# Kernel optimization log

Hardware: AMD Instinct MI355X
Metric: run time of the kernel (lower is better)

The kernel has to match this reference:

```python
import jax, jax.numpy as jnp
import numpy as np

MARGIN = 0.5
CURV = 1.0
B, D = 8192, 128
N_CLASSES = 256


def setup_inputs() -> dict:
    key = jax.random.key(0)
    k1, k2, k3 = jax.random.split(key, 3)
    emb = jax.random.normal(k1, (B, D), dtype=jnp.float32)
    # project onto Poincare ball: random radii in (0, 0.8) so all norms < 1
    radii = 0.8 * jax.random.uniform(k2, (B, 1), dtype=jnp.float32)
    emb = emb / (jnp.linalg.norm(emb, axis=-1, keepdims=True) + 1e-6) * radii
    labels = jax.random.randint(k3, (B,), 0, N_CLASSES, dtype=jnp.int64)
    return {"embeddings": emb, "labels": labels}


def _poincare_dist_matrix(x, c):
    # d(x,y) = arccosh(1 + 2c||x-y||^2 / ((1-c||x||^2)(1-c||y||^2))) / sqrt(c)
    sq = jnp.sum(x * x, axis=-1)                       # (B,)
    gram = x @ x.T                                      # (B,B) GEMM
    d2 = jnp.maximum(sq[:, None] + sq[None, :] - 2.0 * gram, 0.0)
    denom = (1.0 - c * sq)[:, None] * (1.0 - c * sq)[None, :]
    arg = 1.0 + 2.0 * c * d2 / denom
    # clamp slightly above 1: arccosh grad is infinite at 1 (diagonal / identical pts)
    return jnp.arccosh(jnp.maximum(arg, 1.0 + 1e-7)) / jnp.sqrt(c)


def reference(embeddings, labels):
    dist = _poincare_dist_matrix(embeddings, CURV)      # (B,B)
    same = labels[:, None] == labels[None, :]
    eye = jnp.eye(labels.shape[0], dtype=bool)
    pos_mask = same & ~eye
    neg_mask = ~same
    has_pos = jnp.any(pos_mask, axis=1)
    has_neg = jnp.any(neg_mask, axis=1)
    valid = has_pos & has_neg
    d_pos = jnp.max(jnp.where(pos_mask, dist, -jnp.inf), axis=1)
    d_neg = jnp.min(jnp.where(neg_mask, dist, jnp.inf), axis=1)
    d_pos = jnp.where(has_pos, d_pos, 0.0)
    d_neg = jnp.where(has_neg, d_neg, 0.0)
    l = jnp.maximum(d_pos - d_neg + MARGIN, 0.0)
    l = jnp.where(valid, l, 0.0)
    cnt = jnp.sum(valid)
    return jnp.where(cnt > 0, jnp.sum(l) / jnp.maximum(cnt, 1), 0.0)
```

## Files before the change

kernel.cpp:

```cpp
#include <hip/hip_runtime.h>
#include <hip/hip_bf16.h>

typedef __attribute__((ext_vector_type(8))) __bf16 bf16x8;
typedef __attribute__((ext_vector_type(4))) float f32x4;
typedef unsigned short u16;
typedef unsigned int u32;

#define NB 8192
#define ND 128
#define NEGINF (-__builtin_inff())
#define POSINF (__builtin_inff())
#define ENC_NEGINF 0x007FFFFFu
#define ENC_POSINF 0xFF800000u

__device__ inline u16 f2b(float f){
  __hip_bfloat16 h = __float2bfloat16(f);
  return *reinterpret_cast<u16*>(&h);
}
__device__ inline u32 encf(float f){
  u32 b = __float_as_uint(f);
  return b ^ (0x80000000u | (u32)(((int)b) >> 31));
}
__device__ inline float decf(u32 u){
  return __uint_as_float(u ^ (0x80000000u | (u32)((~(int)u) >> 31)));
}

extern "C" __global__ __launch_bounds__(256)
void prep_k(const float* __restrict__ x, const int* __restrict__ lab,
            u16* __restrict__ xb, float4* __restrict__ colp,
            u32* __restrict__ ppos, u32* __restrict__ pneg)
{
  const int tid = blockIdx.x * 256 + threadIdx.x;
  const int row = tid >> 5;
  const int sub = tid & 31;
  const float4 v = reinterpret_cast<const float4*>(x)[row * 32 + sub];
  float s = v.x*v.x + v.y*v.y + v.z*v.z + v.w*v.w;
  #pragma unroll
  for (int m = 1; m < 32; m <<= 1) s += __shfl_xor(s, m, 32);
  ushort4 o;
  o.x = f2b(v.x); o.y = f2b(v.y); o.z = f2b(v.z); o.w = f2b(v.w);
  reinterpret_cast<ushort4*>(xb)[row * 32 + sub] = o;
  if (sub == 0){
    const float p = 1.0f / (1.0f - s);
    colp[row] = make_float4(s, p, s * p, __int_as_float(lab[row]));
  }
  if (sub == 1) ppos[row] = ENC_NEGINF;
  if (sub == 2) pneg[row] = ENC_POSINF;
}

extern "C" __global__ __launch_bounds__(256, 2)
void gram_k(const u16* __restrict__ xb, const float4* __restrict__ colp,
            u32* __restrict__ ppos, u32* __restrict__ pneg)
{
  __shared__ u16 Bt[128 * 128];
  const int wid  = threadIdx.x >> 6;
  const int lane = threadIdx.x & 63;
  const int m16  = lane & 15;
  const int quad = lane >> 4;

  int idx = (int)blockIdx.x;
  int bi = (int)((129.0f - sqrtf((float)(16641 - 8 * idx))) * 0.5f);
  while ((bi + 1) * (129 - (bi + 1)) / 2 <= idx) ++bi;
  while (bi * (129 - bi) / 2 > idx) --bi;
  const int bj = bi + (idx - bi * (129 - bi) / 2);
  const bool diag = (bi == bj);
  const int C0  = bj * 128;
  const int WR0 = bi * 128 + wid * 32;

  #pragma unroll
  for (int c = 0; c < 8; ++c){
    const int cc   = wid * 8 + c;
    const int brow = cc * 4 + quad;
    const int src  = m16 ^ (brow & 15);
    const u16* gsrc = xb + (C0 + brow) * ND + src * 8;
    __builtin_amdgcn_global_load_lds(
        (const __attribute__((address_space(1))) void*)gsrc,
        (__attribute__((address_space(3))) void*)(Bt + cc * 512), 16, 0, 0);
  }

  bf16x8 afrag[2][4];
  #pragma unroll
  for (int mt = 0; mt < 2; ++mt){
    const u16* arow = xb + (WR0 + mt*16 + m16) * ND;
    #pragma unroll
    for (int ks = 0; ks < 4; ++ks)
      afrag[mt][ks] = *reinterpret_cast<const bf16x8*>(arow + ks*32 + quad*8);
  }

  float sqi[8], pi[8]; int labi[8];
  #pragma unroll
  for (int mt = 0; mt < 2; ++mt)
    #pragma unroll
    for (int r = 0; r < 4; ++r){
      const float4 cp = colp[WR0 + mt*16 + quad*4 + r];
      sqi[mt*4+r]  = cp.x;
      pi[mt*4+r]   = cp.y;
      labi[mt*4+r] = __float_as_int(cp.w);
    }

  __syncthreads();

  f32x4 acc[2][8];
  #pragma unroll
  for (int mt = 0; mt < 2; ++mt)
    #pragma unroll
    for (int nt = 0; nt < 8; ++nt){
      f32x4 z = {0.f, 0.f, 0.f, 0.f};
      acc[mt][nt] = z;
    }

  #pragma unroll
  for (int ks = 0; ks < 4; ++ks){
    const int t = ks * 4 + quad;
    #pragma unroll
    for (int nt = 0; nt < 8; ++nt){
      const bf16x8 bfrag = *reinterpret_cast<const bf16x8*>(
          Bt + (nt*16 + m16) * 128 + ((t ^ m16) * 8));
      acc[0][nt] = __builtin_amdgcn_mfma_f32_16x16x32_bf16(afrag[0][ks], bfrag, acc[0][nt], 0, 0, 0);
      acc[1][nt] = __builtin_amdgcn_mfma_f32_16x16x32_bf16(afrag[1][ks], bfrag, acc[1][nt], 0, 0, 0);
    }
  }

  float vpos[8], vneg[8], cpos[8], cneg[8];
  #pragma unroll
  for (int i = 0; i < 8; ++i){
    vpos[i] = NEGINF; vneg[i] = POSINF;
    cpos[i] = NEGINF; cneg[i] = POSINF;
  }

  if (!diag){
    #pragma unroll
    for (int nt = 0; nt < 8; ++nt){
      const float4 cp = colp[C0 + nt*16 + m16];
      const float sqj  = cp.x;
      const float pj   = cp.y;
      const int   labj = __float_as_int(cp.w);
      #pragma unroll
      for (int mt = 0; mt < 2; ++mt)
        #pragma unroll
        for (int r = 0; r < 4; ++r){
          const int i = mt*4 + r;
          const float d2 = fmaf(-2.0f, acc[mt][nt][r], sqi[i] + sqj);
          const float ur = d2 * pj;
          const float uc = d2 * pi[i];
          const bool sm = (labi[i] == labj);
          vpos[i]  = fmaxf(vpos[i],  sm ? ur : NEGINF);
          vneg[i]  = fminf(vneg[i],  sm ? POSINF : ur);
          cpos[nt] = fmaxf(cpos[nt], sm ? uc : NEGINF);
          cneg[nt] = fminf(cneg[nt], sm ? POSINF : uc);
        }
    }
  } else {
    #pragma unroll
    for (int nt = 0; nt < 8; ++nt){
      const float4 cp = colp[C0 + nt*16 + m16];
      const float sqj  = cp.x;
      const float pj   = cp.y;
      const int   labj = __float_as_int(cp.w);
      const int colin  = nt*16 + m16;
      #pragma unroll
      for (int mt = 0; mt < 2; ++mt)
        #pragma unroll
        for (int r = 0; r < 4; ++r){
          const int i = mt*4 + r;
          const float d2 = fmaf(-2.0f, acc[mt][nt][r], sqi[i] + sqj);
          const float ur = d2 * pj;
          const bool sm = (labi[i] == labj);
          const bool dg = (colin == wid*32 + mt*16 + quad*4 + r);
          float ep = sm ? ur : NEGINF;
          ep = dg ? NEGINF : ep;
          vpos[i] = fmaxf(vpos[i], ep);
          vneg[i] = fminf(vneg[i], sm ? POSINF : ur);
        }
    }
  }

  #pragma unroll
  for (int i = 0; i < 8; ++i){
    #pragma unroll
    for (int m = 1; m < 16; m <<= 1){
      vpos[i] = fmaxf(vpos[i], __shfl_xor(vpos[i], m, 16));
      vneg[i] = fminf(vneg[i], __shfl_xor(vneg[i], m, 16));
    }
  }
  if (m16 == 0){
    #pragma unroll
    for (int i = 0; i < 8; ++i){
      const int row = WR0 + (i >> 2)*16 + quad*4 + (i & 3);
      atomicMax(ppos + row, encf(vpos[i]));
      atomicMin(pneg + row, encf(vneg[i]));
    }
  }

  if (!diag){
    #pragma unroll
    for (int nt = 0; nt < 8; ++nt){
      cpos[nt] = fmaxf(cpos[nt], __shfl_xor(cpos[nt], 16));
      cpos[nt] = fmaxf(cpos[nt], __shfl_xor(cpos[nt], 32));
      cneg[nt] = fminf(cneg[nt], __shfl_xor(cneg[nt], 16));
      cneg[nt] = fminf(cneg[nt], __shfl_xor(cneg[nt], 32));
    }
    float* cbP = reinterpret_cast<float*>(Bt);
    float* cbN = cbP + 512;
    __syncthreads();
    if (quad == 0){
      #pragma unroll
      for (int nt = 0; nt < 8; ++nt){
        cbP[wid*128 + nt*16 + m16] = cpos[nt];
        cbN[wid*128 + nt*16 + m16] = cneg[nt];
      }
    }
    __syncthreads();
    if (threadIdx.x < 128){
      const int c = threadIdx.x;
      float P = NEGINF, N = POSINF;
      #pragma unroll
      for (int w = 0; w < 4; ++w){
        P = fmaxf(P, cbP[w*128 + c]);
        N = fminf(N, cbN[w*128 + c]);
      }
      atomicMax(ppos + C0 + c, encf(P));
      atomicMin(pneg + C0 + c, encf(N));
    }
  }
}

extern "C" __global__ __launch_bounds__(128)
void fin1_k(const u32* __restrict__ ppos, const u32* __restrict__ pneg,
            const float4* __restrict__ colp, float2* __restrict__ bpart)
{
  const int row = blockIdx.x * 128 + threadIdx.x;
  const float up = decf(ppos[row]);
  const float un = decf(pneg[row]);
  const bool hp = (up > NEGINF);
  const bool hn = (un < POSINF);
  const float pr = colp[row].y;
  float dp = 0.0f, dn = 0.0f;
  if (hp){ float t = fmaxf(2.0f * up * pr, 1e-7f); dp = log1pf(t + sqrtf(t * (t + 2.0f))); }
  if (hn){ float t = fmaxf(2.0f * un * pr, 1e-7f); dn = log1pf(t + sqrtf(t * (t + 2.0f))); }
  float lsum = (hp && hn) ? fmaxf(dp - dn + 0.5f, 0.0f) : 0.0f;
  float lcnt = (hp && hn) ? 1.0f : 0.0f;
  #pragma unroll
  for (int m = 1; m < 64; m <<= 1){
    lsum += __shfl_xor(lsum, m, 64);
    lcnt += __shfl_xor(lcnt, m, 64);
  }
  __shared__ float2 s_p[2];
  if ((threadIdx.x & 63) == 0) s_p[threadIdx.x >> 6] = make_float2(lsum, lcnt);
  __syncthreads();
  if (threadIdx.x == 0)
    bpart[blockIdx.x] = make_float2(s_p[0].x + s_p[1].x, s_p[0].y + s_p[1].y);
}

extern "C" __global__ __launch_bounds__(64)
void fin2_k(const float2* __restrict__ bpart, float* __restrict__ out)
{
  float2 p = bpart[threadIdx.x];
  float s = p.x, c = p.y;
  #pragma unroll
  for (int m = 1; m < 64; m <<= 1){
    s += __shfl_xor(s, m, 64);
    c += __shfl_xor(c, m, 64);
  }
  if (threadIdx.x == 0) out[0] = (c > 0.0f) ? (s / c) : 0.0f;
}

extern "C" void kernel_launch(void* const* d_in, const int* in_sizes, int n_in,
                              void* d_out, int out_size, void* d_ws, size_t ws_size,
                              hipStream_t stream)
{
  const float* x  = (const float*)d_in[0];
  const int* lab  = (const int*)d_in[1];
  char* ws = (char*)d_ws;
  u16*    xb   = (u16*)ws;
  float4* colp = (float4*)(ws + (size_t)2*1024*1024);
  u32*    ppos = (u32*)(ws + (size_t)2*1024*1024 + 128*1024);
  u32*    pneg = (u32*)(ws + (size_t)2*1024*1024 + 160*1024);
  float2* bpart= (float2*)(ws + (size_t)2*1024*1024 + 192*1024);

  hipLaunchKernelGGL(prep_k, dim3(1024), dim3(256), 0, stream, x, lab, xb, colp, ppos, pneg);
  hipLaunchKernelGGL(gram_k, dim3(2080), dim3(256), 0, stream, xb, colp, ppos, pneg);
  hipLaunchKernelGGL(fin1_k, dim3(64), dim3(128), 0, stream, ppos, pneg, colp, bpart);
  hipLaunchKernelGGL(fin2_k, dim3(1), dim3(64), 0, stream, bpart, (float*)d_out);
}
```

Measured before the change: 105.6 us.

## Sort rows by label so most tiles skip positive-mask work; fuse finalization

Adds a single-block counting sort of rows by class. Embeddings are permuted so each 128-row tile spans a narrow label range, and tile pairs with disjoint class ranges take a cheaper path that tracks only negative minima, without label compares or positive max. The separate finalization kernels are folded into the gram kernel through a last-block-done atomic counter. The MFMA epilogue is split into two halves to reduce register pressure, and occupancy is raised to 3 blocks. This adds a serial single-block sort kernel plus a gather in prep, which adds launch latency and uncoalesced reads.

```diff
diff --git a/kernel.cpp b/kernel.cpp
--- a/kernel.cpp
+++ b/kernel.cpp
@@ -8,6 +8,7 @@
 
 #define NB 8192
 #define ND 128
+#define NBLK 2080
 #define NEGINF (-__builtin_inff())
 #define POSINF (__builtin_inff())
 #define ENC_NEGINF 0x007FFFFFu
@@ -24,48 +25,96 @@
 __device__ inline float decf(u32 u){
   return __uint_as_float(u ^ (0x80000000u | (u32)((~(int)u) >> 31)));
 }
+__device__ inline f32x4 mfma16(bf16x8 a, bf16x8 b, f32x4 c){
+  return __builtin_amdgcn_mfma_f32_16x16x32_bf16(a, b, c, 0, 0, 0);
+}
+
+extern "C" __global__ __launch_bounds__(256)
+void sort_k(const int* __restrict__ lab, int* __restrict__ srcOf,
+            u32* __restrict__ tileCls)
+{
+  __shared__ u32 hist[256], scan[256], startB[256], cnt[256];
+  __shared__ u16 clsS[NB];
+  const int t = threadIdx.x;
+  hist[t] = 0; cnt[t] = 0;
+  __syncthreads();
+  for (int r = t; r < NB; r += 256) atomicAdd(&hist[lab[r]], 1u);
+  __syncthreads();
+  scan[t] = hist[t];
+  __syncthreads();
+  #pragma unroll
+  for (int off = 1; off < 256; off <<= 1){
+    u32 add = (t >= off) ? scan[t - off] : 0u;
+    __syncthreads();
+    scan[t] += add;
+    __syncthreads();
+  }
+  startB[t] = scan[t] - hist[t];
+  __syncthreads();
+  for (int r = t; r < NB; r += 256){
+    const int c = lab[r];
+    const u32 pos = startB[c] + atomicAdd(&cnt[c], 1u);
+    srcOf[pos] = r;
+    clsS[pos] = (u16)c;
+  }
+  __syncthreads();
+  if (t < 64)
+    tileCls[t] = (u32)clsS[t * 128] | ((u32)clsS[t * 128 + 127] << 16);
+}
 
 extern "C" __global__ __launch_bounds__(256)
 void prep_k(const float* __restrict__ x, const int* __restrict__ lab,
+            const int* __restrict__ srcOf,
             u16* __restrict__ xb, float4* __restrict__ colp,
-            u32* __restrict__ ppos, u32* __restrict__ pneg)
+            u32* __restrict__ ppos, u32* __restrict__ pneg,
+            u32* __restrict__ done)
 {
-  const int tid = blockIdx.x * 256 + threadIdx.x;
-  const int row = tid >> 5;
-  const int sub = tid & 31;
-  const float4 v = reinterpret_cast<const float4*>(x)[row * 32 + sub];
-  float s = v.x*v.x + v.y*v.y + v.z*v.z + v.w*v.w;
-  #pragma unroll
-  for (int m = 1; m < 32; m <<= 1) s += __shfl_xor(s, m, 32);
-  ushort4 o;
-  o.x = f2b(v.x); o.y = f2b(v.y); o.z = f2b(v.z); o.w = f2b(v.w);
-  reinterpret_cast<ushort4*>(xb)[row * 32 + sub] = o;
-  if (sub == 0){
-    const float p = 1.0f / (1.0f - s);
-    colp[row] = make_float4(s, p, s * p, __int_as_float(lab[row]));
-  }
-  if (sub == 1) ppos[row] = ENC_NEGINF;
-  if (sub == 2) pneg[row] = ENC_POSINF;
-}
-
-extern "C" __global__ __launch_bounds__(256, 2)
+  const int R0 = blockIdx.x * 128;
+  const int rr  = threadIdx.x >> 5;
+  const int sub = threadIdx.x & 31;
+  for (int it = 0; it < 16; ++it){
+    const int s   = R0 + it * 8 + rr;
+    const int src = srcOf[s];
+    const float4 v = reinterpret_cast<const float4*>(x)[src * 32 + sub];
+    float ss = v.x*v.x + v.y*v.y + v.z*v.z + v.w*v.w;
+    #pragma unroll
+    for (int m = 1; m < 32; m <<= 1) ss += __shfl_xor(ss, m, 32);
+    ushort4 o;
+    o.x = f2b(v.x); o.y = f2b(v.y); o.z = f2b(v.z); o.w = f2b(v.w);
+    reinterpret_cast<ushort4*>(xb)[s * 32 + sub] = o;
+    if (sub == 0){
+      const float p = 1.0f / (1.0f - ss);
+      colp[s] = make_float4(ss, p, ss * p, __int_as_float(lab[src]));
+    }
+  }
+  if (threadIdx.x < 128) ppos[R0 + threadIdx.x] = ENC_NEGINF;
+  else                   pneg[R0 + threadIdx.x - 128] = ENC_POSINF;
+  if (blockIdx.x == 0 && threadIdx.x == 0) *done = 0u;
+}
+
+extern "C" __global__ __launch_bounds__(256, 3)
 void gram_k(const u16* __restrict__ xb, const float4* __restrict__ colp,
-            u32* __restrict__ ppos, u32* __restrict__ pneg)
+            const u32* __restrict__ tileCls,
+            u32* __restrict__ ppos, u32* __restrict__ pneg,
+            u32* __restrict__ done, float* __restrict__ out)
 {
   __shared__ u16 Bt[128 * 128];
+  __shared__ u32 s_last;
   const int wid  = threadIdx.x >> 6;
   const int lane = threadIdx.x & 63;
   const int m16  = lane & 15;
   const int quad = lane >> 4;
 
   int idx = (int)blockIdx.x;
-  int bi = (int)((129.0f - sqrtf((float)(16641 - 8 * idx))) * 0.5f);
-  while ((bi + 1) * (129 - (bi + 1)) / 2 <= idx) ++bi;
-  while (bi * (129 - bi) / 2 > idx) --bi;
-  const int bj = bi + (idx - bi * (129 - bi) / 2);
-  const bool diag = (bi == bj);
+  int bi0 = (int)((129.0f - sqrtf((float)(16641 - 8 * idx))) * 0.5f);
+  while ((bi0 + 1) * (129 - (bi0 + 1)) / 2 <= idx) ++bi0;
+  while (bi0 * (129 - bi0) / 2 > idx) --bi0;
+  const int bi = __builtin_amdgcn_readfirstlane(bi0);
+  const int bj = __builtin_amdgcn_readfirstlane(bi0 + (idx - bi0 * (129 - bi0) / 2));
   const int C0  = bj * 128;
   const int WR0 = bi * 128 + wid * 32;
+  const u32 tci = tileCls[bi], tcj = tileCls[bj];
+  const bool fat = ((tci >> 16) >= (tcj & 0xFFFFu));
 
   #pragma unroll
   for (int c = 0; c < 8; ++c){
@@ -87,182 +136,259 @@
       afrag[mt][ks] = *reinterpret_cast<const bf16x8*>(arow + ks*32 + quad*8);
   }
 
-  float sqi[8], pi[8]; int labi[8];
+  float sqi[8], pi[8];
   #pragma unroll
   for (int mt = 0; mt < 2; ++mt)
     #pragma unroll
     for (int r = 0; r < 4; ++r){
       const float4 cp = colp[WR0 + mt*16 + quad*4 + r];
-      sqi[mt*4+r]  = cp.x;
-      pi[mt*4+r]   = cp.y;
-      labi[mt*4+r] = __float_as_int(cp.w);
-    }
-
-  __syncthreads();
-
-  f32x4 acc[2][8];
-  #pragma unroll
-  for (int mt = 0; mt < 2; ++mt)
+      sqi[mt*4+r] = cp.x;
+      pi[mt*4+r]  = cp.y;
+    }
+
+  __syncthreads();
+
+  if (!fat){
+    float vneg[8], cneg[8];
+    #pragma unroll
+    for (int i = 0; i < 8; ++i){ vneg[i] = POSINF; cneg[i] = POSINF; }
+
+    #pragma unroll
+    for (int half = 0; half < 2; ++half){
+      float4 cpv[4];
+      #pragma unroll
+      for (int nt4 = 0; nt4 < 4; ++nt4)
+        cpv[nt4] = colp[C0 + (half*4 + nt4)*16 + m16];
+      f32x4 acc[2][4];
+      #pragma unroll
+      for (int mt = 0; mt < 2; ++mt)
+        #pragma unroll
+        for (int nt4 = 0; nt4 < 4; ++nt4){
+          f32x4 z = {0.f,0.f,0.f,0.f};
+          acc[mt][nt4] = z;
+        }
+      #pragma unroll
+      for (int ks = 0; ks < 4; ++ks){
+        const int t = ks * 4 + quad;
+        #pragma unroll
+        for (int nt4 = 0; nt4 < 4; ++nt4){
+          const int nt = half*4 + nt4;
+          const bf16x8 bfrag = *reinterpret_cast<const bf16x8*>(
+              Bt + (nt*16 + m16) * 128 + ((t ^ m16) * 8));
+          acc[0][nt4] = mfma16(afrag[0][ks], bfrag, acc[0][nt4]);
+          acc[1][nt4] = mfma16(afrag[1][ks], bfrag, acc[1][nt4]);
+        }
+      }
+      #pragma unroll
+      for (int nt4 = 0; nt4 < 4; ++nt4){
+        const int nt = half*4 + nt4;
+        const float sqj = cpv[nt4].x, pj = cpv[nt4].y;
+        #pragma unroll
+        for (int mt = 0; mt < 2; ++mt)
+          #pragma unroll
+          for (int r = 0; r < 4; ++r){
+            const int i = mt*4 + r;
+            const float d2 = fmaf(-2.0f, acc[mt][nt4][r], sqi[i] + sqj);
+            vneg[i]  = fminf(vneg[i],  d2 * pj);
+            cneg[nt] = fminf(cneg[nt], d2 * pi[i]);
+          }
+      }
+    }
+    #pragma unroll
+    for (int i = 0; i < 8; ++i)
+      #pragma unroll
+      for (int m = 1; m < 16; m <<= 1)
+        vneg[i] = fminf(vneg[i], __shfl_xor(vneg[i], m, 16));
+    if (m16 == 0){
+      #pragma unroll
+      for (int i = 0; i < 8; ++i){
+        const int row = WR0 + (i >> 2)*16 + quad*4 + (i & 3);
+        atomicMin(pneg + row, encf(vneg[i]));
+      }
+    }
     #pragma unroll
     for (int nt = 0; nt < 8; ++nt){
-      f32x4 z = {0.f, 0.f, 0.f, 0.f};
-      acc[mt][nt] = z;
-    }
-
-  #pragma unroll
-  for (int ks = 0; ks < 4; ++ks){
-    const int t = ks * 4 + quad;
-    #pragma unroll
-    for (int nt = 0; nt < 8; ++nt){
-      const bf16x8 bfrag = *reinterpret_cast<const bf16x8*>(
-          Bt + (nt*16 + m16) * 128 + ((t ^ m16) * 8));
-      acc[0][nt] = __builtin_amdgcn_mfma_f32_16x16x32_bf16(afrag[0][ks], bfrag, acc[0][nt], 0, 0, 0);
-      acc[1][nt] = __builtin_amdgcn_mfma_f32_16x16x32_bf16(afrag[1][ks], bfrag, acc[1][nt], 0, 0, 0);
-    }
-  }
-
-  float vpos[8], vneg[8], cpos[8], cneg[8];
-  #pragma unroll
-  for (int i = 0; i < 8; ++i){
-    vpos[i] = NEGINF; vneg[i] = POSINF;
-    cpos[i] = NEGINF; cneg[i] = POSINF;
-  }
-
-  if (!diag){
-    #pragma unroll
-    for (int nt = 0; nt < 8; ++nt){
-      const float4 cp = colp[C0 + nt*16 + m16];
-      const float sqj  = cp.x;
-      const float pj   = cp.y;
-      const int   labj = __float_as_int(cp.w);
-      #pragma unroll
-      for (int mt = 0; mt < 2; ++mt)
-        #pragma unroll
-        for (int r = 0; r < 4; ++r){
-          const int i = mt*4 + r;
-          const float d2 = fmaf(-2.0f, acc[mt][nt][r], sqi[i] + sqj);
-          const float ur = d2 * pj;
-          const float uc = d2 * pi[i];
-          const bool sm = (labi[i] == labj);
-          vpos[i]  = fmaxf(vpos[i],  sm ? ur : NEGINF);
-          vneg[i]  = fminf(vneg[i],  sm ? POSINF : ur);
-          cpos[nt] = fmaxf(cpos[nt], sm ? uc : NEGINF);
-          cneg[nt] = fminf(cneg[nt], sm ? POSINF : uc);
-        }
-    }
-  } else {
-    #pragma unroll
-    for (int nt = 0; nt < 8; ++nt){
-      const float4 cp = colp[C0 + nt*16 + m16];
-      const float sqj  = cp.x;
-      const float pj   = cp.y;
-      const int   labj = __float_as_int(cp.w);
-      const int colin  = nt*16 + m16;
-      #pragma unroll
-      for (int mt = 0; mt < 2; ++mt)
-        #pragma unroll
-        for (int r = 0; r < 4; ++r){
-          const int i = mt*4 + r;
-          const float d2 = fmaf(-2.0f, acc[mt][nt][r], sqi[i] + sqj);
-          const float ur = d2 * pj;
-          const bool sm = (labi[i] == labj);
-          const bool dg = (colin == wid*32 + mt*16 + quad*4 + r);
-          float ep = sm ? ur : NEGINF;
-          ep = dg ? NEGINF : ep;
-          vpos[i] = fmaxf(vpos[i], ep);
-          vneg[i] = fminf(vneg[i], sm ? POSINF : ur);
-        }
-    }
-  }
-
-  #pragma unroll
-  for (int i = 0; i < 8; ++i){
-    #pragma unroll
-    for (int m = 1; m < 16; m <<= 1){
-      vpos[i] = fmaxf(vpos[i], __shfl_xor(vpos[i], m, 16));
-      vneg[i] = fminf(vneg[i], __shfl_xor(vneg[i], m, 16));
-    }
-  }
-  if (m16 == 0){
-    #pragma unroll
-    for (int i = 0; i < 8; ++i){
-      const int row = WR0 + (i >> 2)*16 + quad*4 + (i & 3);
-      atomicMax(ppos + row, encf(vpos[i]));
-      atomicMin(pneg + row, encf(vneg[i]));
-    }
-  }
-
-  if (!diag){
-    #pragma unroll
-    for (int nt = 0; nt < 8; ++nt){
-      cpos[nt] = fmaxf(cpos[nt], __shfl_xor(cpos[nt], 16));
-      cpos[nt] = fmaxf(cpos[nt], __shfl_xor(cpos[nt], 32));
       cneg[nt] = fminf(cneg[nt], __shfl_xor(cneg[nt], 16));
       cneg[nt] = fminf(cneg[nt], __shfl_xor(cneg[nt], 32));
     }
-    float* cbP = reinterpret_cast<float*>(Bt);
-    float* cbN = cbP + 512;
+    float* cbN = reinterpret_cast<float*>(Bt);
     __syncthreads();
     if (quad == 0){
       #pragma unroll
-      for (int nt = 0; nt < 8; ++nt){
-        cbP[wid*128 + nt*16 + m16] = cpos[nt];
+      for (int nt = 0; nt < 8; ++nt)
         cbN[wid*128 + nt*16 + m16] = cneg[nt];
-      }
     }
     __syncthreads();
     if (threadIdx.x < 128){
       const int c = threadIdx.x;
-      float P = NEGINF, N = POSINF;
-      #pragma unroll
-      for (int w = 0; w < 4; ++w){
-        P = fmaxf(P, cbP[w*128 + c]);
-        N = fminf(N, cbN[w*128 + c]);
-      }
-      atomicMax(ppos + C0 + c, encf(P));
+      float N = POSINF;
+      #pragma unroll
+      for (int w = 0; w < 4; ++w) N = fminf(N, cbN[w*128 + c]);
       atomicMin(pneg + C0 + c, encf(N));
     }
-  }
-}
-
-extern "C" __global__ __launch_bounds__(128)
-void fin1_k(const u32* __restrict__ ppos, const u32* __restrict__ pneg,
-            const float4* __restrict__ colp, float2* __restrict__ bpart)
-{
-  const int row = blockIdx.x * 128 + threadIdx.x;
-  const float up = decf(ppos[row]);
-  const float un = decf(pneg[row]);
-  const bool hp = (up > NEGINF);
-  const bool hn = (un < POSINF);
-  const float pr = colp[row].y;
-  float dp = 0.0f, dn = 0.0f;
-  if (hp){ float t = fmaxf(2.0f * up * pr, 1e-7f); dp = log1pf(t + sqrtf(t * (t + 2.0f))); }
-  if (hn){ float t = fmaxf(2.0f * un * pr, 1e-7f); dn = log1pf(t + sqrtf(t * (t + 2.0f))); }
-  float lsum = (hp && hn) ? fmaxf(dp - dn + 0.5f, 0.0f) : 0.0f;
-  float lcnt = (hp && hn) ? 1.0f : 0.0f;
-  #pragma unroll
-  for (int m = 1; m < 64; m <<= 1){
-    lsum += __shfl_xor(lsum, m, 64);
-    lcnt += __shfl_xor(lcnt, m, 64);
-  }
-  __shared__ float2 s_p[2];
-  if ((threadIdx.x & 63) == 0) s_p[threadIdx.x >> 6] = make_float2(lsum, lcnt);
-  __syncthreads();
+  } else {
+    const bool diag = (bi == bj);
+    int labi[8];
+    const float* colpF = reinterpret_cast<const float*>(colp);
+    #pragma unroll
+    for (int mt = 0; mt < 2; ++mt)
+      #pragma unroll
+      for (int r = 0; r < 4; ++r)
+        labi[mt*4+r] = __float_as_int(colpF[(WR0 + mt*16 + quad*4 + r)*4 + 3]);
+
+    float vpos[8], vneg[8], cpos[8], cneg[8];
+    #pragma unroll
+    for (int i = 0; i < 8; ++i){
+      vpos[i] = NEGINF; vneg[i] = POSINF;
+      cpos[i] = NEGINF; cneg[i] = POSINF;
+    }
+
+    #pragma unroll
+    for (int half = 0; half < 2; ++half){
+      float4 cpv[4];
+      #pragma unroll
+      for (int nt4 = 0; nt4 < 4; ++nt4)
+        cpv[nt4] = colp[C0 + (half*4 + nt4)*16 + m16];
+      f32x4 acc[2][4];
+      #pragma unroll
+      for (int mt = 0; mt < 2; ++mt)
+        #pragma unroll
+        for (int nt4 = 0; nt4 < 4; ++nt4){
+          f32x4 z = {0.f,0.f,0.f,0.f};
+          acc[mt][nt4] = z;
+        }
+      #pragma unroll
+      for (int ks = 0; ks < 4; ++ks){
+        const int t = ks * 4 + quad;
+        #pragma unroll
+        for (int nt4 = 0; nt4 < 4; ++nt4){
+          const int nt = half*4 + nt4;
+          const bf16x8 bfrag = *reinterpret_cast<const bf16x8*>(
+              Bt + (nt*16 + m16) * 128 + ((t ^ m16) * 8));
+          acc[0][nt4] = mfma16(afrag[0][ks], bfrag, acc[0][nt4]);
+          acc[1][nt4] = mfma16(afrag[1][ks], bfrag, acc[1][nt4]);
+        }
+      }
+      #pragma unroll
+      for (int nt4 = 0; nt4 < 4; ++nt4){
+        const int nt = half*4 + nt4;
+        const float sqj  = cpv[nt4].x;
+        const float pj   = cpv[nt4].y;
+        const int   labj = __float_as_int(cpv[nt4].w);
+        if (!diag){
+          #pragma unroll
+          for (int mt = 0; mt < 2; ++mt)
+            #pragma unroll
+            for (int r = 0; r < 4; ++r){
+              const int i = mt*4 + r;
+              const float d2 = fmaf(-2.0f, acc[mt][nt4][r], sqi[i] + sqj);
+              const float ur = d2 * pj;
+              const float uc = d2 * pi[i];
+              const bool sm = (labi[i] == labj);
+              vpos[i]  = fmaxf(vpos[i],  sm ? ur : NEGINF);
+              vneg[i]  = fminf(vneg[i],  sm ? POSINF : ur);
+              cpos[nt] = fmaxf(cpos[nt], sm ? uc : NEGINF);
+              cneg[nt] = fminf(cneg[nt], sm ? POSINF : uc);
+            }
+        } else {
+          const int colin = nt*16 + m16;
+          #pragma unroll
+          for (int mt = 0; mt < 2; ++mt)
+            #pragma unroll
+            for (int r = 0; r < 4; ++r){
+              const int i = mt*4 + r;
+              const float d2 = fmaf(-2.0f, acc[mt][nt4][r], sqi[i] + sqj);
+              const float ur = d2 * pj;
+              const bool sm = (labi[i] == labj);
+              const bool dg = (colin == wid*32 + mt*16 + quad*4 + r);
+              float ep = sm ? ur : NEGINF;
+              ep = dg ? NEGINF : ep;
+              vpos[i] = fmaxf(vpos[i], ep);
+              vneg[i] = fminf(vneg[i], sm ? POSINF : ur);
+            }
+        }
+      }
+    }
+    #pragma unroll
+    for (int i = 0; i < 8; ++i)
+      #pragma unroll
+      for (int m = 1; m < 16; m <<= 1){
+        vpos[i] = fmaxf(vpos[i], __shfl_xor(vpos[i], m, 16));
+        vneg[i] = fminf(vneg[i], __shfl_xor(vneg[i], m, 16));
+      }
+    if (m16 == 0){
+      #pragma unroll
+      for (int i = 0; i < 8; ++i){
+        const int row = WR0 + (i >> 2)*16 + quad*4 + (i & 3);
+        atomicMax(ppos + row, encf(vpos[i]));
+        atomicMin(pneg + row, encf(vneg[i]));
+      }
+    }
+    if (!diag){
+      #pragma unroll
+      for (int nt = 0; nt < 8; ++nt){
+        cpos[nt] = fmaxf(cpos[nt], __shfl_xor(cpos[nt], 16));
+        cpos[nt] = fmaxf(cpos[nt], __shfl_xor(cpos[nt], 32));
+        cneg[nt] = fminf(cneg[nt], __shfl_xor(cneg[nt], 16));
+        cneg[nt] = fminf(cneg[nt], __shfl_xor(cneg[nt], 32));
+      }
+      float* cbP = reinterpret_cast<float*>(Bt);
+      float* cbN = cbP + 512;
+      __syncthreads();
+      if (quad == 0){
+        #pragma unroll
+        for (int nt = 0; nt < 8; ++nt){
+          cbP[wid*128 + nt*16 + m16] = cpos[nt];
+          cbN[wid*128 + nt*16 + m16] = cneg[nt];
+        }
+      }
+      __syncthreads();
+      if (threadIdx.x < 128){
+        const int c = threadIdx.x;
+        float P = NEGINF, N = POSINF;
+        #pragma unroll
+        for (int w = 0; w < 4; ++w){
+          P = fmaxf(P, cbP[w*128 + c]);
+          N = fminf(N, cbN[w*128 + c]);
+        }
+        atomicMax(ppos + C0 + c, encf(P));
+        atomicMin(pneg + C0 + c, encf(N));
+      }
+    }
+  }
+
+  __threadfence();
   if (threadIdx.x == 0)
-    bpart[blockIdx.x] = make_float2(s_p[0].x + s_p[1].x, s_p[0].y + s_p[1].y);
-}
-
-extern "C" __global__ __launch_bounds__(64)
-void fin2_k(const float2* __restrict__ bpart, float* __restrict__ out)
-{
-  float2 p = bpart[threadIdx.x];
-  float s = p.x, c = p.y;
-  #pragma unroll
-  for (int m = 1; m < 64; m <<= 1){
-    s += __shfl_xor(s, m, 64);
-    c += __shfl_xor(c, m, 64);
-  }
-  if (threadIdx.x == 0) out[0] = (c > 0.0f) ? (s / c) : 0.0f;
+    s_last = (atomicAdd(done, 1u) == (u32)(NBLK - 1)) ? 1u : 0u;
+  __syncthreads();
+  if (s_last){
+    __threadfence();
+    float lsum = 0.0f, lcnt = 0.0f;
+    for (int r = (int)threadIdx.x; r < NB; r += 256){
+      const float up = decf(atomicMax(ppos + r, 0u));
+      const float un = decf(atomicMin(pneg + r, 0xFFFFFFFFu));
+      const bool hp = (up > NEGINF);
+      const bool hn = (un < POSINF);
+      const float pr = colp[r].y;
+      float dp = 0.0f, dn = 0.0f;
+      if (hp){ float t = fmaxf(2.0f * up * pr, 1e-7f); dp = log1pf(t + sqrtf(t * (t + 2.0f))); }
+      if (hn){ float t = fmaxf(2.0f * un * pr, 1e-7f); dn = log1pf(t + sqrtf(t * (t + 2.0f))); }
+      if (hp && hn){ lsum += fmaxf(dp - dn + 0.5f, 0.0f); lcnt += 1.0f; }
+    }
+    #pragma unroll
+    for (int m = 1; m < 64; m <<= 1){
+      lsum += __shfl_xor(lsum, m, 64);
+      lcnt += __shfl_xor(lcnt, m, 64);
+    }
+    float2* sp = reinterpret_cast<float2*>(Bt);
+    if ((threadIdx.x & 63) == 0) sp[threadIdx.x >> 6] = make_float2(lsum, lcnt);
+    __syncthreads();
+    if (threadIdx.x == 0){
+      const float S = sp[0].x + sp[1].x + sp[2].x + sp[3].x;
+      const float C = sp[0].y + sp[1].y + sp[2].y + sp[3].y;
+      out[0] = (C > 0.0f) ? (S / C) : 0.0f;
+    }
+  }
 }
 
 extern "C" void kernel_launch(void* const* d_in, const int* in_sizes, int n_in,
@@ -272,14 +398,17 @@
   const float* x  = (const float*)d_in[0];
   const int* lab  = (const int*)d_in[1];
   char* ws = (char*)d_ws;
-  u16*    xb   = (u16*)ws;
-  float4* colp = (float4*)(ws + (size_t)2*1024*1024);
-  u32*    ppos = (u32*)(ws + (size_t)2*1024*1024 + 128*1024);
-  u32*    pneg = (u32*)(ws + (size_t)2*1024*1024 + 160*1024);
-  float2* bpart= (float2*)(ws + (size_t)2*1024*1024 + 192*1024);
-
-  hipLaunchKernelGGL(prep_k, dim3(1024), dim3(256), 0, stream, x, lab, xb, colp, ppos, pneg);
-  hipLaunchKernelGGL(gram_k, dim3(2080), dim3(256), 0, stream, xb, colp, ppos, pneg);
-  hipLaunchKernelGGL(fin1_k, dim3(64), dim3(128), 0, stream, ppos, pneg, colp, bpart);
-  hipLaunchKernelGGL(fin2_k, dim3(1), dim3(64), 0, stream, bpart, (float*)d_out);
-}
+  u16*    xb    = (u16*)ws;
+  float4* colp  = (float4*)(ws + (size_t)2*1024*1024);
+  u32*    ppos  = (u32*)(ws + (size_t)2*1024*1024 + 128*1024);
+  u32*    pneg  = (u32*)(ws + (size_t)2*1024*1024 + 160*1024);
+  int*    srcOf = (int*)(ws + (size_t)2*1024*1024 + 192*1024);
+  u32*    tileCls = (u32*)(ws + (size_t)2*1024*1024 + 224*1024);
+  u32*    done  = (u32*)(ws + (size_t)2*1024*1024 + 225*1024);
+
+  hipLaunchKernelGGL(sort_k, dim3(1), dim3(256), 0, stream, lab, srcOf, tileCls);
+  hipLaunchKernelGGL(prep_k, dim3(64), dim3(256), 0, stream,
+                     x, lab, srcOf, xb, colp, ppos, pneg, done);
+  hipLaunchKernelGGL(gram_k, dim3(NBLK), dim3(256), 0, stream,
+                     xb, colp, tileCls, ppos, pneg, done, (float*)d_out);
+}
```

After: 259.2 us. 2.45x slower.

## Fuse prep, gram and finalize kernels into one launch with last-block reduction

Applied to the files above, without the earlier changes.

Replaces the four-kernel pipeline (bf16 prep, gram, two finalize passes) with a memset plus a single fused kernel. Each tile block converts its own fp32 rows to bf16 and computes norms on the fly, and the last block to finish does the final loss reduction. The scaled distance is now folded symmetrically as d2*pi*pj, and the atomics are skipped for infinite values. This removes launch overhead and the intermediate bf16 buffer, at the cost of redundant conversion and norm work for every tile and a serial finalize done by one block.

```diff
diff --git a/kernel.cpp b/kernel.cpp
--- a/kernel.cpp
+++ b/kernel.cpp
@@ -7,16 +7,10 @@
 typedef unsigned int u32;
 
 #define NB 8192
-#define ND 128
+#define NBLK 2080
 #define NEGINF (-__builtin_inff())
 #define POSINF (__builtin_inff())
-#define ENC_NEGINF 0x007FFFFFu
-#define ENC_POSINF 0xFF800000u
-
-__device__ inline u16 f2b(float f){
-  __hip_bfloat16 h = __float2bfloat16(f);
-  return *reinterpret_cast<u16*>(&h);
-}
+
 __device__ inline u32 encf(float f){
   u32 b = __float_as_uint(f);
   return b ^ (0x80000000u | (u32)(((int)b) >> 31));
@@ -24,81 +18,92 @@
 __device__ inline float decf(u32 u){
   return __uint_as_float(u ^ (0x80000000u | (u32)((~(int)u) >> 31)));
 }
-
-extern "C" __global__ __launch_bounds__(256)
-void prep_k(const float* __restrict__ x, const int* __restrict__ lab,
-            u16* __restrict__ xb, float4* __restrict__ colp,
-            u32* __restrict__ ppos, u32* __restrict__ pneg)
-{
-  const int tid = blockIdx.x * 256 + threadIdx.x;
-  const int row = tid >> 5;
-  const int sub = tid & 31;
-  const float4 v = reinterpret_cast<const float4*>(x)[row * 32 + sub];
-  float s = v.x*v.x + v.y*v.y + v.z*v.z + v.w*v.w;
-  #pragma unroll
-  for (int m = 1; m < 32; m <<= 1) s += __shfl_xor(s, m, 32);
-  ushort4 o;
-  o.x = f2b(v.x); o.y = f2b(v.y); o.z = f2b(v.z); o.w = f2b(v.w);
-  reinterpret_cast<ushort4*>(xb)[row * 32 + sub] = o;
-  if (sub == 0){
-    const float p = 1.0f / (1.0f - s);
-    colp[row] = make_float4(s, p, s * p, __int_as_float(lab[row]));
-  }
-  if (sub == 1) ppos[row] = ENC_NEGINF;
-  if (sub == 2) pneg[row] = ENC_POSINF;
+__device__ inline f32x4 mfma16(bf16x8 a, bf16x8 b, f32x4 c){
+  return __builtin_amdgcn_mfma_f32_16x16x32_bf16(a, b, c, 0, 0, 0);
+}
+__device__ inline ushort4 cvt4(float4 a){
+  union { ushort4 s; __hip_bfloat162 h[2]; } u;
+  u.h[0] = __float22bfloat162_rn(make_float2(a.x, a.y));
+  u.h[1] = __float22bfloat162_rn(make_float2(a.z, a.w));
+  return u.s;
+}
+__device__ inline bf16x8 cvt8(float4 a, float4 b){
+  union { bf16x8 v; __hip_bfloat162 h[4]; } u;
+  u.h[0] = __float22bfloat162_rn(make_float2(a.x, a.y));
+  u.h[1] = __float22bfloat162_rn(make_float2(a.z, a.w));
+  u.h[2] = __float22bfloat162_rn(make_float2(b.x, b.y));
+  u.h[3] = __float22bfloat162_rn(make_float2(b.z, b.w));
+  return u.v;
 }
 
 extern "C" __global__ __launch_bounds__(256, 2)
-void gram_k(const u16* __restrict__ xb, const float4* __restrict__ colp,
-            u32* __restrict__ ppos, u32* __restrict__ pneg)
+void fused_k(const float* __restrict__ x, const int* __restrict__ lab,
+             u32* __restrict__ pm, u32* __restrict__ nm,
+             u32* __restrict__ done, float* __restrict__ out)
 {
   __shared__ u16 Bt[128 * 128];
-  const int wid  = threadIdx.x >> 6;
-  const int lane = threadIdx.x & 63;
+  __shared__ float sqA[128], pA[128], sqB[128], pB[128];
+  __shared__ int labA[128], labB[128];
+  __shared__ u32 s_last;
+  __shared__ float2 s_fin[4];
+
+  const int tid  = threadIdx.x;
+  const int wid  = tid >> 6;
+  const int lane = tid & 63;
   const int m16  = lane & 15;
   const int quad = lane >> 4;
 
   int idx = (int)blockIdx.x;
-  int bi = (int)((129.0f - sqrtf((float)(16641 - 8 * idx))) * 0.5f);
-  while ((bi + 1) * (129 - (bi + 1)) / 2 <= idx) ++bi;
-  while (bi * (129 - bi) / 2 > idx) --bi;
-  const int bj = bi + (idx - bi * (129 - bi) / 2);
+  int bi0 = (int)((129.0f - sqrtf((float)(16641 - 8 * idx))) * 0.5f);
+  while ((bi0 + 1) * (129 - (bi0 + 1)) / 2 <= idx) ++bi0;
+  while (bi0 * (129 - bi0) / 2 > idx) --bi0;
+  const int bi = bi0;
+  const int bj = bi0 + (idx - bi0 * (129 - bi0) / 2);
   const bool diag = (bi == bj);
-  const int C0  = bj * 128;
-  const int WR0 = bi * 128 + wid * 32;
-
-  #pragma unroll
-  for (int c = 0; c < 8; ++c){
-    const int cc   = wid * 8 + c;
-    const int brow = cc * 4 + quad;
-    const int src  = m16 ^ (brow & 15);
-    const u16* gsrc = xb + (C0 + brow) * ND + src * 8;
-    __builtin_amdgcn_global_load_lds(
-        (const __attribute__((address_space(1))) void*)gsrc,
-        (__attribute__((address_space(3))) void*)(Bt + cc * 512), 16, 0, 0);
+  const int R0 = bi * 128, C0 = bj * 128;
+  const int WR0 = R0 + wid * 32;
+
+  const int rr = tid >> 5, sub = tid & 31;
+  for (int pp = 0; pp < 16; ++pp){
+    const int r = pp * 8 + rr;
+    const float4 va = reinterpret_cast<const float4*>(x)[(R0 + r) * 32 + sub];
+    float sa = va.x*va.x + va.y*va.y + va.z*va.z + va.w*va.w;
+    #pragma unroll
+    for (int m = 1; m < 32; m <<= 1) sa += __shfl_xor(sa, m, 32);
+    const float4 vb = reinterpret_cast<const float4*>(x)[(C0 + r) * 32 + sub];
+    float sb = vb.x*vb.x + vb.y*vb.y + vb.z*vb.z + vb.w*vb.w;
+    #pragma unroll
+    for (int m = 1; m < 32; m <<= 1) sb += __shfl_xor(sb, m, 32);
+    if (sub == 0){
+      sqA[r] = sa; pA[r] = 1.0f / (1.0f - sa);
+      sqB[r] = sb; pB[r] = 1.0f / (1.0f - sb);
+    }
+    if (sub == 1) labA[r] = lab[R0 + r];
+    if (sub == 2) labB[r] = lab[C0 + r];
+    reinterpret_cast<ushort4*>(Bt)[r*32 + (((sub>>1) ^ (r & 15)) << 1) + (sub & 1)] = cvt4(vb);
   }
 
   bf16x8 afrag[2][4];
   #pragma unroll
   for (int mt = 0; mt < 2; ++mt){
-    const u16* arow = xb + (WR0 + mt*16 + m16) * ND;
+    const float4* ar = reinterpret_cast<const float4*>(x) + (size_t)(WR0 + mt*16 + m16) * 32;
     #pragma unroll
     for (int ks = 0; ks < 4; ++ks)
-      afrag[mt][ks] = *reinterpret_cast<const bf16x8*>(arow + ks*32 + quad*8);
-  }
+      afrag[mt][ks] = cvt8(ar[ks*8 + quad*2], ar[ks*8 + quad*2 + 1]);
+  }
+
+  __syncthreads();
 
   float sqi[8], pi[8]; int labi[8];
   #pragma unroll
   for (int mt = 0; mt < 2; ++mt)
     #pragma unroll
     for (int r = 0; r < 4; ++r){
-      const float4 cp = colp[WR0 + mt*16 + quad*4 + r];
-      sqi[mt*4+r]  = cp.x;
-      pi[mt*4+r]   = cp.y;
-      labi[mt*4+r] = __float_as_int(cp.w);
-    }
-
-  __syncthreads();
+      const int rl = wid*32 + mt*16 + quad*4 + r;
+      sqi[mt*4+r]  = sqA[rl];
+      pi[mt*4+r]   = pA[rl];
+      labi[mt*4+r] = labA[rl];
+    }
 
   f32x4 acc[2][8];
   #pragma unroll
@@ -108,7 +113,6 @@
       f32x4 z = {0.f, 0.f, 0.f, 0.f};
       acc[mt][nt] = z;
     }
-
   #pragma unroll
   for (int ks = 0; ks < 4; ++ks){
     const int t = ks * 4 + quad;
@@ -116,8 +120,8 @@
     for (int nt = 0; nt < 8; ++nt){
       const bf16x8 bfrag = *reinterpret_cast<const bf16x8*>(
           Bt + (nt*16 + m16) * 128 + ((t ^ m16) * 8));
-      acc[0][nt] = __builtin_amdgcn_mfma_f32_16x16x32_bf16(afrag[0][ks], bfrag, acc[0][nt], 0, 0, 0);
-      acc[1][nt] = __builtin_amdgcn_mfma_f32_16x16x32_bf16(afrag[1][ks], bfrag, acc[1][nt], 0, 0, 0);
+      acc[0][nt] = mfma16(afrag[0][ks], bfrag, acc[0][nt]);
+      acc[1][nt] = mfma16(afrag[1][ks], bfrag, acc[1][nt]);
     }
   }
 
@@ -127,68 +131,57 @@
     vpos[i] = NEGINF; vneg[i] = POSINF;
     cpos[i] = NEGINF; cneg[i] = POSINF;
   }
-
-  if (!diag){
-    #pragma unroll
-    for (int nt = 0; nt < 8; ++nt){
-      const float4 cp = colp[C0 + nt*16 + m16];
-      const float sqj  = cp.x;
-      const float pj   = cp.y;
-      const int   labj = __float_as_int(cp.w);
+  #pragma unroll
+  for (int nt = 0; nt < 8; ++nt){
+    const float sqj  = sqB[nt*16 + m16];
+    const float pj   = pB[nt*16 + m16];
+    const int   labj = labB[nt*16 + m16];
+    if (!diag){
       #pragma unroll
       for (int mt = 0; mt < 2; ++mt)
         #pragma unroll
         for (int r = 0; r < 4; ++r){
           const int i = mt*4 + r;
           const float d2 = fmaf(-2.0f, acc[mt][nt][r], sqi[i] + sqj);
-          const float ur = d2 * pj;
-          const float uc = d2 * pi[i];
+          const float w  = d2 * (pi[i] * pj);
           const bool sm = (labi[i] == labj);
-          vpos[i]  = fmaxf(vpos[i],  sm ? ur : NEGINF);
-          vneg[i]  = fminf(vneg[i],  sm ? POSINF : ur);
-          cpos[nt] = fmaxf(cpos[nt], sm ? uc : NEGINF);
-          cneg[nt] = fminf(cneg[nt], sm ? POSINF : uc);
+          vpos[i]  = fmaxf(vpos[i],  sm ? w : NEGINF);
+          vneg[i]  = fminf(vneg[i],  sm ? POSINF : w);
+          cpos[nt] = fmaxf(cpos[nt], sm ? w : NEGINF);
+          cneg[nt] = fminf(cneg[nt], sm ? POSINF : w);
         }
-    }
-  } else {
-    #pragma unroll
-    for (int nt = 0; nt < 8; ++nt){
-      const float4 cp = colp[C0 + nt*16 + m16];
-      const float sqj  = cp.x;
-      const float pj   = cp.y;
-      const int   labj = __float_as_int(cp.w);
-      const int colin  = nt*16 + m16;
+    } else {
+      const int colin = nt*16 + m16;
       #pragma unroll
       for (int mt = 0; mt < 2; ++mt)
         #pragma unroll
         for (int r = 0; r < 4; ++r){
           const int i = mt*4 + r;
           const float d2 = fmaf(-2.0f, acc[mt][nt][r], sqi[i] + sqj);
-          const float ur = d2 * pj;
+          const float w  = d2 * (pi[i] * pj);
           const bool sm = (labi[i] == labj);
           const bool dg = (colin == wid*32 + mt*16 + quad*4 + r);
-          float ep = sm ? ur : NEGINF;
+          float ep = sm ? w : NEGINF;
           ep = dg ? NEGINF : ep;
           vpos[i] = fmaxf(vpos[i], ep);
-          vneg[i] = fminf(vneg[i], sm ? POSINF : ur);
+          vneg[i] = fminf(vneg[i], sm ? POSINF : w);
         }
     }
   }
 
   #pragma unroll
-  for (int i = 0; i < 8; ++i){
+  for (int i = 0; i < 8; ++i)
     #pragma unroll
     for (int m = 1; m < 16; m <<= 1){
       vpos[i] = fmaxf(vpos[i], __shfl_xor(vpos[i], m, 16));
       vneg[i] = fminf(vneg[i], __shfl_xor(vneg[i], m, 16));
     }
-  }
   if (m16 == 0){
     #pragma unroll
     for (int i = 0; i < 8; ++i){
       const int row = WR0 + (i >> 2)*16 + quad*4 + (i & 3);
-      atomicMax(ppos + row, encf(vpos[i]));
-      atomicMin(pneg + row, encf(vneg[i]));
+      if (vpos[i] > NEGINF) atomicMax(pm + row, encf(vpos[i]));
+      if (vneg[i] < POSINF) atomicMax(nm + row, ~encf(vneg[i]));
     }
   }
 
@@ -211,58 +204,45 @@
       }
     }
     __syncthreads();
-    if (threadIdx.x < 128){
-      const int c = threadIdx.x;
+    if (tid < 128){
       float P = NEGINF, N = POSINF;
       #pragma unroll
       for (int w = 0; w < 4; ++w){
-        P = fmaxf(P, cbP[w*128 + c]);
-        N = fminf(N, cbN[w*128 + c]);
+        P = fmaxf(P, cbP[w*128 + tid]);
+        N = fminf(N, cbN[w*128 + tid]);
       }
-      atomicMax(ppos + C0 + c, encf(P));
-      atomicMin(pneg + C0 + c, encf(N));
-    }
-  }
-}
-
-extern "C" __global__ __launch_bounds__(128)
-void fin1_k(const u32* __restrict__ ppos, const u32* __restrict__ pneg,
-            const float4* __restrict__ colp, float2* __restrict__ bpart)
-{
-  const int row = blockIdx.x * 128 + threadIdx.x;
-  const float up = decf(ppos[row]);
-  const float un = decf(pneg[row]);
-  const bool hp = (up > NEGINF);
-  const bool hn = (un < POSINF);
-  const float pr = colp[row].y;
-  float dp = 0.0f, dn = 0.0f;
-  if (hp){ float t = fmaxf(2.0f * up * pr, 1e-7f); dp = log1pf(t + sqrtf(t * (t + 2.0f))); }
-  if (hn){ float t = fmaxf(2.0f * un * pr, 1e-7f); dn = log1pf(t + sqrtf(t * (t + 2.0f))); }
-  float lsum = (hp && hn) ? fmaxf(dp - dn + 0.5f, 0.0f) : 0.0f;
-  float lcnt = (hp && hn) ? 1.0f : 0.0f;
-  #pragma unroll
-  for (int m = 1; m < 64; m <<= 1){
-    lsum += __shfl_xor(lsum, m, 64);
-    lcnt += __shfl_xor(lcnt, m, 64);
-  }
-  __shared__ float2 s_p[2];
-  if ((threadIdx.x & 63) == 0) s_p[threadIdx.x >> 6] = make_float2(lsum, lcnt);
+      if (P > NEGINF) atomicMax(pm + C0 + tid, encf(P));
+      if (N < POSINF) atomicMax(nm + C0 + tid, ~encf(N));
+    }
+  }
+
   __syncthreads();
-  if (threadIdx.x == 0)
-    bpart[blockIdx.x] = make_float2(s_p[0].x + s_p[1].x, s_p[0].y + s_p[1].y);
-}
-
-extern "C" __global__ __launch_bounds__(64)
-void fin2_k(const float2* __restrict__ bpart, float* __restrict__ out)
-{
-  float2 p = bpart[threadIdx.x];
-  float s = p.x, c = p.y;
-  #pragma unroll
-  for (int m = 1; m < 64; m <<= 1){
-    s += __shfl_xor(s, m, 64);
-    c += __shfl_xor(c, m, 64);
-  }
-  if (threadIdx.x == 0) out[0] = (c > 0.0f) ? (s / c) : 0.0f;
+  if (tid == 0)
+    s_last = (atomicAdd(done, 1u) == (u32)(NBLK - 1)) ? 1u : 0u;
+  __syncthreads();
+  if (s_last){
+    float lsum = 0.0f, lcnt = 0.0f;
+    for (int r = tid; r < NB; r += 256){
+      const u32 pe = atomicMax(pm + r, 0u);
+      const u32 ne = atomicMax(nm + r, 0u);
+      float dp = 0.0f, dn = 0.0f;
+      if (pe){ float t = fmaxf(2.0f * decf(pe),  1e-7f); dp = log1pf(t + sqrtf(t * (t + 2.0f))); }
+      if (ne){ float t = fmaxf(2.0f * decf(~ne), 1e-7f); dn = log1pf(t + sqrtf(t * (t + 2.0f))); }
+      if (pe && ne){ lsum += fmaxf(dp - dn + 0.5f, 0.0f); lcnt += 1.0f; }
+    }
+    #pragma unroll
+    for (int m = 1; m < 64; m <<= 1){
+      lsum += __shfl_xor(lsum, m, 64);
+      lcnt += __shfl_xor(lcnt, m, 64);
+    }
+    if (lane == 0) s_fin[wid] = make_float2(lsum, lcnt);
+    __syncthreads();
+    if (tid == 0){
+      const float S = s_fin[0].x + s_fin[1].x + s_fin[2].x + s_fin[3].x;
+      const float C = s_fin[0].y + s_fin[1].y + s_fin[2].y + s_fin[3].y;
+      out[0] = (C > 0.0f) ? (S / C) : 0.0f;
+    }
+  }
 }
 
 extern "C" void kernel_launch(void* const* d_in, const int* in_sizes, int n_in,
@@ -272,14 +252,11 @@
   const float* x  = (const float*)d_in[0];
   const int* lab  = (const int*)d_in[1];
   char* ws = (char*)d_ws;
-  u16*    xb   = (u16*)ws;
-  float4* colp = (float4*)(ws + (size_t)2*1024*1024);
-  u32*    ppos = (u32*)(ws + (size_t)2*1024*1024 + 128*1024);
-  u32*    pneg = (u32*)(ws + (size_t)2*1024*1024 + 160*1024);
-  float2* bpart= (float2*)(ws + (size_t)2*1024*1024 + 192*1024);
-
-  hipLaunchKernelGGL(prep_k, dim3(1024), dim3(256), 0, stream, x, lab, xb, colp, ppos, pneg);
-  hipLaunchKernelGGL(gram_k, dim3(2080), dim3(256), 0, stream, xb, colp, ppos, pneg);
-  hipLaunchKernelGGL(fin1_k, dim3(64), dim3(128), 0, stream, ppos, pneg, colp, bpart);
-  hipLaunchKernelGGL(fin2_k, dim3(1), dim3(64), 0, stream, bpart, (float*)d_out);
-}
+  u32* pm   = (u32*)ws;
+  u32* nm   = (u32*)(ws + 32*1024);
+  u32* done = (u32*)(ws + 64*1024);
+
+  hipMemsetAsync(ws, 0, 64*1024 + 64, stream);
+  hipLaunchKernelGGL(fused_k, dim3(NBLK), dim3(256), 0, stream,
+                     x, lab, pm, nm, done, (float*)d_out);
+}
```

Result: slower. 165.0 us (+56.2%).
